# Optimization experiments

Hardware: AMD Instinct MI355X
Metric: run time of the kernel (lower is better)

Reference implementation:

```python
import jax, jax.numpy as jnp
import numpy as np

T, B, S = 50, 64, 100
H, C = 512, 512
V_TGT, V_EXT = 32000, 5000
UNK = 0  # ext_dict.stoi[UNK_WORD]


def setup_inputs() -> dict:
    key = jax.random.key(0)
    ks = jax.random.split(key, 8)
    return {
        "hidden": jax.random.normal(ks[0], (T, B, H), jnp.float32),
        "dec_rnn_output": jax.random.normal(ks[1], (T, B, H), jnp.float32),
        "concat_c": jax.random.normal(ks[2], (T, B, H + C), jnp.float32),
        "attn": jax.random.uniform(ks[3], (T, B, S), jnp.float32),
        "copy_to_ext": jax.random.randint(ks[4], (S, B), 0, V_EXT, jnp.int64),
        "W": jax.random.normal(ks[5], (V_TGT, H), jnp.float32) * 0.02,
        "b": jnp.zeros((V_TGT,), jnp.float32),
        "Wc": jax.random.normal(ks[6], (1, H), jnp.float32) * 0.02,
        "bc": jnp.zeros((1,), jnp.float32),
    }


def _safe_log(v):
    return jnp.log(jnp.clip(v, 0.001, 1.0 - 0.001))


def reference(hidden, dec_rnn_output, concat_c, attn, copy_to_ext, W, b, Wc, bc):
    # standard softmax over tgt vocab
    logits = jnp.einsum("tbh,vh->tbv", hidden, W) + b          # [T,B,V_TGT]
    prob_log = jax.nn.log_softmax(logits, axis=-1)
    # copy gate p(z) from decoder hidden (copy_prb == 'hidden')
    copy = jax.nn.sigmoid(jnp.einsum("tbh,oh->tbo", dec_rnn_output, Wc) + bc)  # [T,B,1]
    mul_attn = attn * (1.0 - copy)                              # [T,B,S]
    # onehot+bmm == masked scatter-add of attn mass into ext-vocab bins
    mask = (copy_to_ext != UNK).astype(mul_attn.dtype)          # [S,B]
    aw = mul_attn * mask.T[None]                                # [T,B,S]

    def scatter_one(a_ts, idx_s):  # a_ts [T,S], idx_s [S]
        return jnp.zeros((T, V_EXT), a_ts.dtype).at[:, idx_s].add(a_ts)

    ext_copy_prob = jax.vmap(scatter_one, in_axes=(1, 1), out_axes=1)(aw, copy_to_ext)  # [T,B,V_EXT]
    ext_copy_prob_log = _safe_log(ext_copy_prob)
    return jnp.concatenate([prob_log, ext_copy_prob_log], axis=-1)  # [T,B,V_TGT+V_EXT]
```

## Files before the change

kernel.cpp:

```cpp
#include <hip/hip_runtime.h>
#include <hip/hip_bf16.h>

#define TT 50
#define BB 64
#define SS 100
#define HH 512
#define VT 32000
#define VE 5000
#define LDC 37000
#define MROWS 3200
#define NTILE 250
#define TSTR 136
#define STG_COLS 22016

typedef __bf16 bf16x8 __attribute__((ext_vector_type(8)));
typedef float f32x4 __attribute__((ext_vector_type(4)));

__device__ __forceinline__ ushort f2bf(float f) {
    unsigned u = __float_as_uint(f);
    u += 0x7fffu + ((u >> 16) & 1u);
    return (ushort)(u >> 16);
}
__device__ __forceinline__ float bflo(unsigned u) { return __uint_as_float(u << 16); }
__device__ __forceinline__ float bfhi(unsigned u) { return __uint_as_float(u & 0xffff0000u); }

__global__ void convert_kernel(const float* __restrict__ W, const float* __restrict__ hid,
                               ushort* __restrict__ wsB, ushort* __restrict__ wsA) {
    int g = blockIdx.x * 256 + threadIdx.x;
    const int WG = 4096000;
    float4 v;
    ushort* dst;
    if (g < WG) {
        v = ((const float4*)W)[g];
        dst = wsB + 4 * (size_t)g;
    } else {
        int h = g - WG;
        v = ((const float4*)hid)[h];
        dst = wsA + 4 * (size_t)h;
    }
    ushort4 o;
    o.x = f2bf(v.x); o.y = f2bf(v.y); o.z = f2bf(v.z); o.w = f2bf(v.w);
    *(ushort4*)dst = o;
}

__global__ void gemm_kernel(const ushort* __restrict__ A, const ushort* __restrict__ B,
                            const float* __restrict__ bias, ushort* __restrict__ outu,
                            float* __restrict__ pm, float* __restrict__ ps) {
    __shared__ char smem[34816];
    const int tid  = threadIdx.x;
    const int w    = tid >> 6;
    const int lane = tid & 63;
    const int wr   = w >> 1, wc = w & 1;
    const int brow = blockIdx.y * 128;
    const int bcol = blockIdx.x * 128;
    const int lr   = lane & 15;
    const int kg   = lane >> 4;

    char* ldsAb = smem;
    char* ldsBb = smem + 16384;
    ushort* tileT = (ushort*)smem;

    f32x4 acc[4][4];
#pragma unroll
    for (int m = 0; m < 4; ++m)
#pragma unroll
        for (int n = 0; n < 4; ++n)
            acc[m][n] = (f32x4){0.f, 0.f, 0.f, 0.f};

    for (int kt = 0; kt < 8; ++kt) {
        __syncthreads();
#pragma unroll
        for (int j = 0; j < 4; ++j) {
            int c = tid + j * 256;
            int row = c >> 3, kc = c & 7;
            int kcs = kc ^ (row & 7);
            const ushort* srcA = A + (size_t)(brow + row) * HH + kt * 64 + kcs * 8;
            __builtin_amdgcn_global_load_lds(
                (const __attribute__((address_space(1))) void*)srcA,
                (__attribute__((address_space(3))) void*)(ldsAb + c * 16),
                16, 0, 0);
            const ushort* srcB = B + (size_t)(bcol + row) * HH + kt * 64 + kcs * 8;
            __builtin_amdgcn_global_load_lds(
                (const __attribute__((address_space(1))) void*)srcB,
                (__attribute__((address_space(3))) void*)(ldsBb + c * 16),
                16, 0, 0);
        }
        __syncthreads();

#pragma unroll
        for (int s = 0; s < 2; ++s) {
            bf16x8 af[4], bfr[4];
            int xof = ((s * 4 + kg) ^ (lr & 7)) << 4;
#pragma unroll
            for (int m = 0; m < 4; ++m)
                af[m] = *(const bf16x8*)(ldsAb + (wr * 64 + m * 16 + lr) * 128 + xof);
#pragma unroll
            for (int n = 0; n < 4; ++n)
                bfr[n] = *(const bf16x8*)(ldsBb + (wc * 64 + n * 16 + lr) * 128 + xof);
#pragma unroll
            for (int m = 0; m < 4; ++m)
#pragma unroll
                for (int n = 0; n < 4; ++n)
                    acc[m][n] = __builtin_amdgcn_mfma_f32_16x16x32_bf16(af[m], bfr[n], acc[m][n], 0, 0, 0);
        }
    }
    __syncthreads();

#pragma unroll
    for (int n = 0; n < 4; ++n) {
        int col = wc * 64 + n * 16 + lr;
        float bv = bias[bcol + col];
#pragma unroll
        for (int m = 0; m < 4; ++m) {
            int row0 = wr * 64 + m * 16 + kg * 4;
#pragma unroll
            for (int r = 0; r < 4; ++r)
                tileT[(row0 + r) * TSTR + col] = f2bf(acc[m][n][r] + bv);
        }
    }
    __syncthreads();

#pragma unroll
    for (int it = 0; it < 8; ++it) {
        int idx = it * 256 + tid;
        int row = idx >> 4, ch = idx & 15;
        uint4 v = *(const uint4*)(&tileT[row * TSTR + ch * 8]);
        *(uint4*)(outu + (size_t)(brow + row) * 74000 + 42000 + bcol + ch * 8) = v;
    }

    {
        int prow = tid >> 1, half = tid & 1;
        const ushort* trow = &tileT[prow * TSTR + half * 64];
        uint4 vv[8];
#pragma unroll
        for (int i = 0; i < 8; ++i) vv[i] = *(const uint4*)(trow + i * 8);
        float mx = -1e30f;
#pragma unroll
        for (int i = 0; i < 8; ++i) {
            mx = fmaxf(mx, fmaxf(fmaxf(bflo(vv[i].x), bfhi(vv[i].x)), fmaxf(bflo(vv[i].y), bfhi(vv[i].y))));
            mx = fmaxf(mx, fmaxf(fmaxf(bflo(vv[i].z), bfhi(vv[i].z)), fmaxf(bflo(vv[i].w), bfhi(vv[i].w))));
        }
        float sx = 0.f;
#pragma unroll
        for (int i = 0; i < 8; ++i) {
            sx += __expf(bflo(vv[i].x) - mx) + __expf(bfhi(vv[i].x) - mx)
                + __expf(bflo(vv[i].y) - mx) + __expf(bfhi(vv[i].y) - mx)
                + __expf(bflo(vv[i].z) - mx) + __expf(bfhi(vv[i].z) - mx)
                + __expf(bflo(vv[i].w) - mx) + __expf(bfhi(vv[i].w) - mx);
        }
        float om = __shfl_xor(mx, 1), os = __shfl_xor(sx, 1);
        float M = fmaxf(mx, om);
        float S = sx * __expf(mx - M) + os * __expf(om - M);
        if (half == 0) {
            pm[(size_t)blockIdx.x * MROWS + brow + prow] = M;
            ps[(size_t)blockIdx.x * MROWS + brow + prow] = S;
        }
    }
}

__global__ __launch_bounds__(512) void norm_ext_kernel(float* __restrict__ out,
                                                       const float* __restrict__ pm,
                                                       const float* __restrict__ ps,
                                                       const float* __restrict__ dec,
                                                       const float* __restrict__ wc,
                                                       const float* __restrict__ bcp,
                                                       const float* __restrict__ attn,
                                                       const int* __restrict__ cte) {
    const int r = blockIdx.x;
    const int t = threadIdx.x;
    __shared__ float sm[8], ssum[8];
    __shared__ float lse_sh, csh;
    __shared__ ushort stg[STG_COLS];
    __shared__ float bins[VE];

    float m = -1e30f, s = 0.f;
    if (t < NTILE) {
        m = pm[(size_t)t * MROWS + r];
        s = ps[(size_t)t * MROWS + r];
    }
    for (int off = 1; off < 64; off <<= 1) {
        float om = __shfl_xor(m, off), os = __shfl_xor(s, off);
        float nm = fmaxf(m, om);
        s = s * __expf(m - nm) + os * __expf(om - nm);
        m = nm;
    }
    int w = t >> 6, lane = t & 63;
    if (lane == 0) { sm[w] = m; ssum[w] = s; }

    {
        float part = dec[(size_t)r * HH + t] * wc[t];
        for (int off = 1; off < 64; off <<= 1) part += __shfl_xor(part, off);
        if (lane == 0) ssum[w] += 0.f, sm[w] += 0.f;
        __shared__ float red[8];
        if (lane == 0) red[w] = part;
        if (t == 0) csh = 0.f;
        const uint4* src = (const uint4*)((const ushort*)out + (size_t)r * 74000 + 42000);
        uint4* dstl = (uint4*)stg;
        for (int i = t; i < STG_COLS / 8; i += 512) dstl[i] = src[i];
        for (int v = t; v < VE; v += 512) bins[v] = 0.f;
        __syncthreads();
        if (t == 0) {
            float M = sm[0], S = ssum[0];
            for (int i = 1; i < 8; ++i) {
                float nm = fmaxf(M, sm[i]);
                S = S * __expf(M - nm) + ssum[i] * __expf(sm[i] - nm);
                M = nm;
            }
            lse_sh = M + __logf(S);
            float g = red[0] + red[1] + red[2] + red[3]
                    + red[4] + red[5] + red[6] + red[7] + bcp[0];
            csh = 1.f / (1.f + __expf(-g));
        }
    }
    __syncthreads();
    const float l = lse_sh;

    const uint4* gsrc = (const uint4*)((const ushort*)out + (size_t)r * 74000 + 42000);
    const uint4* lsrc = (const uint4*)stg;
    float4* orow = (float4*)(out + (size_t)r * LDC);
    for (int i = t; i < VT / 8; i += 512) {
        uint4 v = (i < STG_COLS / 8) ? lsrc[i] : gsrc[i];
        float4 a, b;
        a.x = bflo(v.x) - l; a.y = bfhi(v.x) - l;
        a.z = bflo(v.y) - l; a.w = bfhi(v.y) - l;
        b.x = bflo(v.z) - l; b.y = bfhi(v.z) - l;
        b.z = bflo(v.w) - l; b.w = bfhi(v.w) - l;
        orow[2 * i]     = a;
        orow[2 * i + 1] = b;
    }

    if (t < SS) {
        float aw = attn[(size_t)r * SS + t] * (1.f - csh);
        int idx = cte[t * BB + (r & 63)];
        if (idx != 0) atomicAdd(&bins[idx], aw);
    }
    __syncthreads();

    float4* eo = (float4*)(out + (size_t)r * LDC + VT);
    for (int v = t; v < VE / 4; v += 512) {
        float4 x;
        x.x = __logf(fminf(fmaxf(bins[4 * v + 0], 0.001f), 0.999f));
        x.y = __logf(fminf(fmaxf(bins[4 * v + 1], 0.001f), 0.999f));
        x.z = __logf(fminf(fmaxf(bins[4 * v + 2], 0.001f), 0.999f));
        x.w = __logf(fminf(fmaxf(bins[4 * v + 3], 0.001f), 0.999f));
        eo[v] = x;
    }
}

extern "C" void kernel_launch(void* const* d_in, const int* in_sizes, int n_in,
                              void* d_out, int out_size, void* d_ws, size_t ws_size,
                              hipStream_t stream) {
    const float* hidden = (const float*)d_in[0];
    const float* dec    = (const float*)d_in[1];
    const float* attn   = (const float*)d_in[3];
    const int*   cte    = (const int*)d_in[4];
    const float* W      = (const float*)d_in[5];
    const float* bias   = (const float*)d_in[6];
    const float* Wc     = (const float*)d_in[7];
    const float* bc     = (const float*)d_in[8];
    float* out = (float*)d_out;

    ushort* wsB = (ushort*)d_ws;
    ushort* wsA = wsB + (size_t)VT * HH;
    float*  pm  = (float*)(wsA + (size_t)MROWS * HH);
    float*  ps  = pm + (size_t)NTILE * MROWS;

    convert_kernel<<<17600, 256, 0, stream>>>(W, hidden, wsB, wsA);
    gemm_kernel<<<dim3(NTILE, 25), 256, 0, stream>>>(wsA, wsB, bias, (ushort*)out, pm, ps);
    norm_ext_kernel<<<MROWS, 512, 0, stream>>>(out, pm, ps, dec, Wc, bc, attn, cte);
}
```

Before: 372.1 us.

## Double-buffer GEMM LDS loads and drop LDS staging in norm kernel

The GEMM main loop moves from 8 single-buffered K=64 steps to 16 double-buffered K=32 steps. The next tile's global-to-LDS loads are issued before waiting on the current one, using explicit vmcnt waits and barriers, so load latency overlaps MFMA work. The XOR swizzle on the LDS layout is dropped, which may add bank conflicts on the fragment reads. The normalization kernel now runs with 256 threads and no large LDS staging copy of the bf16 logits. It converts in place from global memory, with periodic block barriers to keep in-place reads ahead of writes, which cuts LDS use and should raise occupancy.

```diff
diff --git a/kernel.cpp b/kernel.cpp
--- a/kernel.cpp
+++ b/kernel.cpp
@@ -11,7 +11,6 @@
 #define MROWS 3200
 #define NTILE 250
 #define TSTR 136
-#define STG_COLS 22016
 
 typedef __bf16 bf16x8 __attribute__((ext_vector_type(8)));
 typedef float f32x4 __attribute__((ext_vector_type(4)));
@@ -43,9 +42,12 @@
     *(ushort4*)dst = o;
 }
 
-__global__ void gemm_kernel(const ushort* __restrict__ A, const ushort* __restrict__ B,
-                            const float* __restrict__ bias, ushort* __restrict__ outu,
-                            float* __restrict__ pm, float* __restrict__ ps) {
+__global__ __launch_bounds__(256) void gemm_kernel(const ushort* __restrict__ A,
+                                                   const ushort* __restrict__ B,
+                                                   const float* __restrict__ bias,
+                                                   ushort* __restrict__ outu,
+                                                   float* __restrict__ pm,
+                                                   float* __restrict__ ps) {
     __shared__ char smem[34816];
     const int tid  = threadIdx.x;
     const int w    = tid >> 6;
@@ -56,9 +58,10 @@
     const int lr   = lane & 15;
     const int kg   = lane >> 4;
 
-    char* ldsAb = smem;
-    char* ldsBb = smem + 16384;
     ushort* tileT = (ushort*)smem;
+    const int c0 = tid, c1 = tid + 256;
+    const int r0 = c0 >> 2, k0 = c0 & 3;
+    const int r1 = c1 >> 2, k1 = c1 & 3;
 
     f32x4 acc[4][4];
 #pragma unroll
@@ -67,43 +70,56 @@
         for (int n = 0; n < 4; ++n)
             acc[m][n] = (f32x4){0.f, 0.f, 0.f, 0.f};
 
-    for (int kt = 0; kt < 8; ++kt) {
-        __syncthreads();
-#pragma unroll
-        for (int j = 0; j < 4; ++j) {
-            int c = tid + j * 256;
-            int row = c >> 3, kc = c & 7;
-            int kcs = kc ^ (row & 7);
-            const ushort* srcA = A + (size_t)(brow + row) * HH + kt * 64 + kcs * 8;
-            __builtin_amdgcn_global_load_lds(
-                (const __attribute__((address_space(1))) void*)srcA,
-                (__attribute__((address_space(3))) void*)(ldsAb + c * 16),
-                16, 0, 0);
-            const ushort* srcB = B + (size_t)(bcol + row) * HH + kt * 64 + kcs * 8;
-            __builtin_amdgcn_global_load_lds(
-                (const __attribute__((address_space(1))) void*)srcB,
-                (__attribute__((address_space(3))) void*)(ldsBb + c * 16),
-                16, 0, 0);
-        }
-        __syncthreads();
-
-#pragma unroll
-        for (int s = 0; s < 2; ++s) {
-            bf16x8 af[4], bfr[4];
-            int xof = ((s * 4 + kg) ^ (lr & 7)) << 4;
-#pragma unroll
-            for (int m = 0; m < 4; ++m)
-                af[m] = *(const bf16x8*)(ldsAb + (wr * 64 + m * 16 + lr) * 128 + xof);
+#define STAGE(buf, kt)                                                                      \
+    do {                                                                                    \
+        char* bA = smem + (buf) * 8192;                                                     \
+        char* bB = smem + 16384 + (buf) * 8192;                                             \
+        __builtin_amdgcn_global_load_lds(                                                   \
+            (const __attribute__((address_space(1))) void*)(A + (size_t)(brow + r0) * HH + (kt) * 32 + k0 * 8), \
+            (__attribute__((address_space(3))) void*)(bA + c0 * 16), 16, 0, 0);             \
+        __builtin_amdgcn_global_load_lds(                                                   \
+            (const __attribute__((address_space(1))) void*)(A + (size_t)(brow + r1) * HH + (kt) * 32 + k1 * 8), \
+            (__attribute__((address_space(3))) void*)(bA + c1 * 16), 16, 0, 0);             \
+        __builtin_amdgcn_global_load_lds(                                                   \
+            (const __attribute__((address_space(1))) void*)(B + (size_t)(bcol + r0) * HH + (kt) * 32 + k0 * 8), \
+            (__attribute__((address_space(3))) void*)(bB + c0 * 16), 16, 0, 0);             \
+        __builtin_amdgcn_global_load_lds(                                                   \
+            (const __attribute__((address_space(1))) void*)(B + (size_t)(bcol + r1) * HH + (kt) * 32 + k1 * 8), \
+            (__attribute__((address_space(3))) void*)(bB + c1 * 16), 16, 0, 0);             \
+    } while (0)
+
+    STAGE(0, 0);
+    for (int kt = 0; kt < 16; ++kt) {
+        const int cur = kt & 1;
+        if (kt < 15) {
+            STAGE(cur ^ 1, kt + 1);
+            asm volatile("s_waitcnt vmcnt(4)" ::: "memory");
+        } else {
+            asm volatile("s_waitcnt vmcnt(0)" ::: "memory");
+        }
+        __builtin_amdgcn_sched_barrier(0);
+        __builtin_amdgcn_s_barrier();
+        __builtin_amdgcn_sched_barrier(0);
+
+        const char* pa = smem + cur * 8192;
+        const char* pb = smem + 16384 + cur * 8192;
+        bf16x8 af[4], bfr[4];
+#pragma unroll
+        for (int m = 0; m < 4; ++m)
+            af[m] = *(const bf16x8*)(pa + (wr * 64 + m * 16 + lr) * 64 + kg * 16);
+#pragma unroll
+        for (int n = 0; n < 4; ++n)
+            bfr[n] = *(const bf16x8*)(pb + (wc * 64 + n * 16 + lr) * 64 + kg * 16);
+#pragma unroll
+        for (int m = 0; m < 4; ++m)
 #pragma unroll
             for (int n = 0; n < 4; ++n)
-                bfr[n] = *(const bf16x8*)(ldsBb + (wc * 64 + n * 16 + lr) * 128 + xof);
-#pragma unroll
-            for (int m = 0; m < 4; ++m)
-#pragma unroll
-                for (int n = 0; n < 4; ++n)
-                    acc[m][n] = __builtin_amdgcn_mfma_f32_16x16x32_bf16(af[m], bfr[n], acc[m][n], 0, 0, 0);
-        }
-    }
+                acc[m][n] = __builtin_amdgcn_mfma_f32_16x16x32_bf16(af[m], bfr[n], acc[m][n], 0, 0, 0);
+
+        __builtin_amdgcn_sched_barrier(0);
+        __builtin_amdgcn_s_barrier();
+    }
+#undef STAGE
     __syncthreads();
 
 #pragma unroll
@@ -158,7 +174,7 @@
     }
 }
 
-__global__ __launch_bounds__(512) void norm_ext_kernel(float* __restrict__ out,
+__global__ __launch_bounds__(256) void norm_ext_kernel(float* __restrict__ out,
                                                        const float* __restrict__ pm,
                                                        const float* __restrict__ ps,
                                                        const float* __restrict__ dec,
@@ -168,9 +184,9 @@
                                                        const int* __restrict__ cte) {
     const int r = blockIdx.x;
     const int t = threadIdx.x;
-    __shared__ float sm[8], ssum[8];
+    const int w = t >> 6, lane = t & 63;
+    __shared__ float sm[4], ssv[4], red[4];
     __shared__ float lse_sh, csh;
-    __shared__ ushort stg[STG_COLS];
     __shared__ float bins[VE];
 
     float m = -1e30f, s = 0.f;
@@ -184,60 +200,58 @@
         s = s * __expf(m - nm) + os * __expf(om - nm);
         m = nm;
     }
-    int w = t >> 6, lane = t & 63;
-    if (lane == 0) { sm[w] = m; ssum[w] = s; }
+    if (lane == 0) { sm[w] = m; ssv[w] = s; }
 
     {
-        float part = dec[(size_t)r * HH + t] * wc[t];
+        float part = dec[(size_t)r * HH + t] * wc[t]
+                   + dec[(size_t)r * HH + t + 256] * wc[t + 256];
         for (int off = 1; off < 64; off <<= 1) part += __shfl_xor(part, off);
-        if (lane == 0) ssum[w] += 0.f, sm[w] += 0.f;
-        __shared__ float red[8];
         if (lane == 0) red[w] = part;
-        if (t == 0) csh = 0.f;
-        const uint4* src = (const uint4*)((const ushort*)out + (size_t)r * 74000 + 42000);
-        uint4* dstl = (uint4*)stg;
-        for (int i = t; i < STG_COLS / 8; i += 512) dstl[i] = src[i];
-        for (int v = t; v < VE; v += 512) bins[v] = 0.f;
-        __syncthreads();
-        if (t == 0) {
-            float M = sm[0], S = ssum[0];
-            for (int i = 1; i < 8; ++i) {
-                float nm = fmaxf(M, sm[i]);
-                S = S * __expf(M - nm) + ssum[i] * __expf(sm[i] - nm);
-                M = nm;
-            }
-            lse_sh = M + __logf(S);
-            float g = red[0] + red[1] + red[2] + red[3]
-                    + red[4] + red[5] + red[6] + red[7] + bcp[0];
-            csh = 1.f / (1.f + __expf(-g));
-        }
+    }
+    for (int v = t; v < VE; v += 256) bins[v] = 0.f;
+    __syncthreads();
+
+    if (t == 0) {
+        float M = sm[0], S = ssv[0];
+        for (int i = 1; i < 4; ++i) {
+            float nm = fmaxf(M, sm[i]);
+            S = S * __expf(M - nm) + ssv[i] * __expf(sm[i] - nm);
+            M = nm;
+        }
+        lse_sh = M + __logf(S);
+        float g = red[0] + red[1] + red[2] + red[3] + bcp[0];
+        csh = 1.f / (1.f + __expf(-g));
     }
     __syncthreads();
     const float l = lse_sh;
-
-    const uint4* gsrc = (const uint4*)((const ushort*)out + (size_t)r * 74000 + 42000);
-    const uint4* lsrc = (const uint4*)stg;
-    float4* orow = (float4*)(out + (size_t)r * LDC);
-    for (int i = t; i < VT / 8; i += 512) {
-        uint4 v = (i < STG_COLS / 8) ? lsrc[i] : gsrc[i];
-        float4 a, b;
-        a.x = bflo(v.x) - l; a.y = bfhi(v.x) - l;
-        a.z = bflo(v.y) - l; a.w = bfhi(v.y) - l;
-        b.x = bflo(v.z) - l; b.y = bfhi(v.z) - l;
-        b.z = bflo(v.w) - l; b.w = bfhi(v.w) - l;
-        orow[2 * i]     = a;
-        orow[2 * i + 1] = b;
-    }
+    const float c = csh;
 
     if (t < SS) {
-        float aw = attn[(size_t)r * SS + t] * (1.f - csh);
+        float aw = attn[(size_t)r * SS + t] * (1.f - c);
         int idx = cte[t * BB + (r & 63)];
         if (idx != 0) atomicAdd(&bins[idx], aw);
     }
+
+    const uint4* gsrc = (const uint4*)((const ushort*)out + (size_t)r * 74000 + 42000);
+    float4* orow = (float4*)(out + (size_t)r * LDC);
+    for (int n = 0; n < 16; ++n) {
+        int i = t + 256 * n;
+        if (i < VT / 8) {
+            uint4 v = gsrc[i];
+            float4 a, b;
+            a.x = bflo(v.x) - l; a.y = bfhi(v.x) - l;
+            a.z = bflo(v.y) - l; a.w = bfhi(v.y) - l;
+            b.x = bflo(v.z) - l; b.y = bfhi(v.z) - l;
+            b.z = bflo(v.w) - l; b.w = bfhi(v.w) - l;
+            orow[2 * i]     = a;
+            orow[2 * i + 1] = b;
+        }
+        if ((n & 1) == 1) __syncthreads();
+    }
     __syncthreads();
 
     float4* eo = (float4*)(out + (size_t)r * LDC + VT);
-    for (int v = t; v < VE / 4; v += 512) {
+    for (int v = t; v < VE / 4; v += 256) {
         float4 x;
         x.x = __logf(fminf(fmaxf(bins[4 * v + 0], 0.001f), 0.999f));
         x.y = __logf(fminf(fmaxf(bins[4 * v + 1], 0.001f), 0.999f));
@@ -267,5 +281,5 @@
 
     convert_kernel<<<17600, 256, 0, stream>>>(W, hidden, wsB, wsA);
     gemm_kernel<<<dim3(NTILE, 25), 256, 0, stream>>>(wsA, wsB, bias, (ushort*)out, pm, ps);
-    norm_ext_kernel<<<MROWS, 512, 0, stream>>>(out, pm, ps, dec, Wc, bc, attn, cte);
-}
+    norm_ext_kernel<<<MROWS, 256, 0, stream>>>(out, pm, ps, dec, Wc, bc, attn, cte);
+}
```

Result: faster. 349.6 us (-6.1%).
